# Kernel tuning notes

Hardware: AMD Instinct MI355X
Metric: run time of the kernel (lower is better)

## Reference

```python
import jax, jax.numpy as jnp
from jax import lax
import numpy as np

N_QUBITS = 8
Q_DEPTH = 10
DIM = 256  # 2**8

# basis-state bit table; wire 0 = most-significant bit (PennyLane convention)
_bits = ((np.arange(DIM)[:, None] >> (N_QUBITS - 1 - np.arange(N_QUBITS))) & 1)
# phase layer: S on even wires (phase i), T on odd wires (phase e^{i pi/4})
_ph = np.where(np.arange(N_QUBITS) % 2 == 0, 1j, np.exp(1j * np.pi / 4))
_diag = np.prod(np.power(_ph[None, :], _bits), axis=1)
# entangling_layer_3 CZ pattern
_cz = np.ones(DIM)
for i, j in [(0, 1), (2, 3), (4, 5), (6, 7), (1, 2), (3, 4), (5, 6)]:
    _cz = _cz * ((-1.0) ** (_bits[:, i] * _bits[:, j]))
DIAG = jnp.asarray((_diag * _cz).astype(np.complex64))  # phase+CZ layer fused diagonal
ZSIGNS = jnp.asarray((1 - 2 * _bits).astype(np.float32))  # [256, 8] PauliZ eigenvalues
H_GATE = jnp.asarray((np.array([[1.0, 1.0], [1.0, -1.0]]) / np.sqrt(2.0)).astype(np.complex64))
X_GATE = jnp.asarray(np.array([[0.0, 1.0], [1.0, 0.0]]).astype(np.complex64))
EYE2 = jnp.eye(2, dtype=jnp.complex64)
BN_EPS = 1e-5


def apply_1q(state, U, w):
    """Apply 2x2 gate U on wire w; state: [B, 2,2,...,2]."""
    state = jnp.moveaxis(state, w + 1, -1)
    state = jnp.matmul(state, U.T)
    return jnp.moveaxis(state, -1, w + 1)


def quantum_net(features, q_params):
    """Batched statevector sim of quantum_net_3. features [B,256], q_params [80] -> [B,8]."""
    f = features / jnp.linalg.norm(features, axis=1, keepdims=True)
    state = f.astype(jnp.complex64).reshape((-1,) + (2,) * N_QUBITS)
    for w in range(N_QUBITS):
        state = apply_1q(state, H_GATE, w)
    qw = q_params.reshape(Q_DEPTH, N_QUBITS)
    for layer in range(Q_DEPTH):
        for w in range(N_QUBITS):
            t = qw[layer, w]
            c = jnp.cos(t / 2).astype(jnp.complex64)
            s = jnp.sin(t / 2).astype(jnp.complex64)
            U = c * EYE2 + (-1j) * s * X_GATE  # RX(t)
            state = apply_1q(state, U, w)
        flat = state.reshape(-1, DIM) * DIAG  # phase layer + CZ entangling (diagonal)
        state = flat.reshape((-1,) + (2,) * N_QUBITS)
    sv = state.reshape(-1, DIM)
    probs = sv.real ** 2 + sv.imag ** 2
    return probs @ ZSIGNS  # [B, 8] expval(PauliZ_i)


def conv2d(x, w, b):
    y = lax.conv_general_dilated(x, w, (1, 1), 'SAME', dimension_numbers=('NCHW', 'OIHW', 'NCHW'))
    return y + b[None, :, None, None]


def bn(x, gamma, beta, mean, var):  # eval-mode BatchNorm2d
    inv = gamma / jnp.sqrt(var + BN_EPS)
    return x * inv[None, :, None, None] + (beta - mean * inv)[None, :, None, None]


def maxpool2(x):
    return lax.reduce_window(x, -jnp.inf, lax.max, (1, 1, 2, 2), (1, 1, 2, 2), 'VALID')


def setup_inputs() -> dict:
    key = jax.random.key(0)
    ks = jax.random.split(key, 16)
    B = 1024
    return {
        'x': jax.random.normal(ks[0], (B, 1, 28, 28), dtype=jnp.float32),
        'conv1_w': 0.1 * jax.random.normal(ks[1], (32, 1, 3, 3), dtype=jnp.float32),
        'conv1_b': jnp.zeros((32,), jnp.float32),
        'bn1_gamma': jnp.ones((32,), jnp.float32),
        'bn1_beta': jnp.zeros((32,), jnp.float32),
        'bn1_mean': jnp.zeros((32,), jnp.float32),
        'bn1_var': jnp.ones((32,), jnp.float32),
        'conv2_w': 0.05 * jax.random.normal(ks[2], (64, 32, 3, 3), dtype=jnp.float32),
        'conv2_b': jnp.zeros((64,), jnp.float32),
        'bn2_gamma': jnp.ones((64,), jnp.float32),
        'bn2_beta': jnp.zeros((64,), jnp.float32),
        'bn2_mean': jnp.zeros((64,), jnp.float32),
        'bn2_var': jnp.ones((64,), jnp.float32),
        'fc_w': 0.01 * jax.random.normal(ks[3], (256, 64 * 7 * 7), dtype=jnp.float32),
        'fc_b': jnp.zeros((256,), jnp.float32),
        'q_params': 0.1 * jax.random.normal(ks[4], (Q_DEPTH * N_QUBITS,), dtype=jnp.float32),
        'p1_w': 0.01 * jax.random.normal(ks[5], (128, 8), dtype=jnp.float32),
        'p1_b': jnp.zeros((128,), jnp.float32),
        'p2_w': 0.01 * jax.random.normal(ks[6], (64, 128), dtype=jnp.float32),
        'p2_b': jnp.zeros((64,), jnp.float32),
        'p3_w': 0.01 * jax.random.normal(ks[7], (10, 64), dtype=jnp.float32),
        'p3_b': jnp.zeros((10,), jnp.float32),
    }


def reference(x, conv1_w, conv1_b, bn1_gamma, bn1_beta, bn1_mean, bn1_var,
              conv2_w, conv2_b, bn2_gamma, bn2_beta, bn2_mean, bn2_var,
              fc_w, fc_b, q_params, p1_w, p1_b, p2_w, p2_b, p3_w, p3_b):
    h = maxpool2(jax.nn.relu(bn(conv2d(x, conv1_w, conv1_b), bn1_gamma, bn1_beta, bn1_mean, bn1_var)))
    h = maxpool2(jax.nn.relu(bn(conv2d(h, conv2_w, conv2_b), bn2_gamma, bn2_beta, bn2_mean, bn2_var)))
    h = h.reshape(h.shape[0], -1)  # [B, 64*7*7]
    feats = jnp.tanh(h @ fc_w.T + fc_b)  # [B, 256]
    q = quantum_net(feats, q_params)  # [B, 8]
    z = jax.nn.relu(q @ p1_w.T + p1_b)  # dropout = identity (eval)
    z = jax.nn.relu(z @ p2_w.T + p2_b)
    return z @ p3_w.T + p3_b
```

## Files before the change

kernel.cpp:

```cpp
#include <hip/hip_runtime.h>
#include <math.h>


#define B_SZ 1024

#define OFF_FCWP   0
#define OFF_W2F    802816
#define OFF_SC2    821600
#define OFF_SH2    821664
#define OFF_H1     821728
#define OFF_H2P    7244256

#define KSPLIT_FC 14
#define TS 40

typedef __attribute__((ext_vector_type(8))) short s16x8;
typedef __attribute__((ext_vector_type(4))) float f32x4;

__constant__ float C_COS8[8] = {1.f, 0.70710678f, 0.f, -0.70710678f, -1.f, -0.70710678f, 0.f, 0.70710678f};
__constant__ float C_SIN8[8] = {0.f, 0.70710678f, 1.f, 0.70710678f, 0.f, -0.70710678f, -1.f, -0.70710678f};

__device__ __forceinline__ unsigned short bf16_rne(float f) {
  unsigned u = __float_as_uint(f);
  unsigned r = u + 0x7FFFu + ((u >> 16) & 1u);
  return (unsigned short)(r >> 16);
}
__device__ __forceinline__ int div14(int m) {
  return __float2int_rz((float)m * 0.07142858f);
}

__global__ __launch_bounds__(256) void fused_front_kernel(
    const float* __restrict__ x, const float* __restrict__ c1w, const float* __restrict__ c1b,
    const float* __restrict__ bn1g, const float* __restrict__ bn1b, const float* __restrict__ bn1m,
    const float* __restrict__ bn1v,
    const float* __restrict__ c2w,
    const float* __restrict__ bn2g, const float* __restrict__ bn2b, const float* __restrict__ bn2m,
    const float* __restrict__ bn2v, const float* __restrict__ c2b,
    const float* __restrict__ fc_w,
    float* __restrict__ ws) {
  const int blk = blockIdx.x, tid = threadIdx.x;
  __shared__ float smem[3136];

  if (blk >= 1024) {
    if (blk < 1280) {
      const int n = blk - 1024;
      const float* src = fc_w + n * 3136;
      for (int i = tid; i < 3136; i += 256) smem[i] = src[i];
      __syncthreads();
      unsigned short* us = (unsigned short*)ws;
      const int nt = n >> 4, nl = n & 15;
      for (int k = tid; k < 3136; k += 256) {
        float v = smem[(k & 63) * 49 + (k >> 6)];
        unsigned short hi = bf16_rne(v);
        unsigned short lo = bf16_rne(v - __uint_as_float((unsigned)hi << 16));
        const int lane_ = ((k >> 3) & 3) * 16 + nl;
        const int base = (((k >> 5) * 16 + nt) * 2) * 512 + lane_ * 8 + (k & 7);
        us[base] = hi;
        us[base + 512] = lo;
      }
    } else if (blk < 1424) {
      int g = (blk - 1280) * 256 + tid;
      int j = g & 7, L = (g >> 3) & 63, rest = g >> 9;
      int h = rest & 1; rest >>= 1;
      int t = rest % 9, w = rest / 9;
      int occ = w * 16 + (L & 15);
      int ic  = (L >> 4) * 8 + j;
      float v = c2w[occ * 288 + ic * 9 + t];
      unsigned short hi = bf16_rne(v);
      unsigned short res = hi;
      if (h) res = bf16_rne(v - __uint_as_float((unsigned)hi << 16));
      ((unsigned short*)(ws + OFF_W2F))[g] = res;
    } else {
      if (tid < 64) {
        float inv = bn2g[tid] / sqrtf(bn2v[tid] + 1e-5f);
        ws[OFF_SC2 + tid] = inv;
        ws[OFF_SH2 + tid] = c2b[tid] * inv + bn2b[tid] - bn2m[tid] * inv;
      }
    }
    return;
  }

  const int b = blk;
  float (*xs)[32] = (float (*)[32])smem;
  float* w1s  = smem + 960;
  float* sc1s = smem + 1248;
  float* sh1s = smem + 1280;
  float* h1 = ws + OFF_H1;

  if (tid < 240) ((float4*)smem)[tid] = make_float4(0.f, 0.f, 0.f, 0.f);
  __syncthreads();
  const float* xb = x + b * 784;
  for (int i = tid; i < 784; i += 256) {
    int y = i / 28, c = i - y * 28;
    xs[y + 1][c + 1] = xb[i];
  }
  for (int i = tid; i < 288; i += 256) w1s[i] = c1w[(i & 31) * 9 + (i >> 5)];
  if (tid < 32) {
    float inv = bn1g[tid] / sqrtf(bn1v[tid] + 1e-5f);
    sc1s[tid] = inv;
    sh1s[tid] = c1b[tid] * inv + bn1b[tid] - bn1m[tid] * inv;
  }
  __syncthreads();

  for (int t = tid; t < 448; t += 256) {
    const int oc = t & 31, py = t >> 5;
    float wv[9];
#pragma unroll
    for (int k = 0; k < 9; ++k) wv[k] = w1s[k * 32 + oc];
    float acc0[28], acc1[28];
#pragma unroll
    for (int j = 0; j < 28; ++j) { acc0[j] = 0.f; acc1[j] = 0.f; }
#pragma unroll
    for (int r = 0; r < 4; ++r) {
      const int pr = 2 * py + r;
      float row[32];
#pragma unroll
      for (int q = 0; q < 8; ++q) {
        float4 v = *(const float4*)&xs[pr][4 * q];
        row[4 * q] = v.x; row[4 * q + 1] = v.y; row[4 * q + 2] = v.z; row[4 * q + 3] = v.w;
      }
      if (r <= 2) {
#pragma unroll
        for (int kx = 0; kx < 3; ++kx) {
          const float w = wv[r * 3 + kx];
#pragma unroll
          for (int xx = 0; xx < 28; ++xx) acc0[xx] = fmaf(row[xx + kx], w, acc0[xx]);
        }
      }
      if (r >= 1) {
#pragma unroll
        for (int kx = 0; kx < 3; ++kx) {
          const float w = wv[(r - 1) * 3 + kx];
#pragma unroll
          for (int xx = 0; xx < 28; ++xx) acc1[xx] = fmaf(row[xx + kx], w, acc1[xx]);
        }
      }
    }
    const float sc = sc1s[oc], sh = sh1s[oc];
    float* dst = h1 + b * 6272 + oc * 196 + py * 14;
#pragma unroll
    for (int px = 0; px < 14; ++px) {
      float v0 = fmaxf(fmaf(acc0[2 * px], sc, sh), 0.f);
      float v1 = fmaxf(fmaf(acc0[2 * px + 1], sc, sh), 0.f);
      float v2 = fmaxf(fmaf(acc1[2 * px], sc, sh), 0.f);
      float v3 = fmaxf(fmaf(acc1[2 * px + 1], sc, sh), 0.f);
      dst[px] = fmaxf(fmaxf(v0, v1), fmaxf(v2, v3));
    }
  }
}

__global__ __launch_bounds__(256, 2) void conv2_kernel(
    const float* __restrict__ h1, const float* __restrict__ w2f_f,
    const float* __restrict__ sc2, const float* __restrict__ sh2,
    unsigned short* __restrict__ h2hi, unsigned short* __restrict__ h2lo) {
  const int b = blockIdx.x, tid = threadIdx.x;
  const int lane = tid & 63, w = tid >> 6;

  __shared__ unsigned char lds_raw[50176];
  unsigned short* tile_hi = (unsigned short*)lds_raw;
  unsigned short* tile_lo = (unsigned short*)(lds_raw + 21760);
  float* conv_out = (float*)lds_raw;

  const unsigned short* w2f = (const unsigned short*)w2f_f;
  s16x8 bf[9][2];
#pragma unroll
  for (int t = 0; t < 9; ++t)
#pragma unroll
    for (int h = 0; h < 2; ++h)
      bf[t][h] = *(const s16x8*)&w2f[(((w * 9 + t) * 2 + h) << 9) + lane * 8];

  {
    float4* z = (float4*)lds_raw;
    for (int i = tid; i < 2720; i += 256) z[i] = make_float4(0.f, 0.f, 0.f, 0.f);
  }
  __syncthreads();

  if (tid < 196) {
    const int y = div14(tid), x = tid - y * 14;
    const int sp = ((y + 1) * 16 + (x + 1)) * TS;
    const float* src = h1 + b * 6272 + tid;
#pragma unroll
    for (int c = 0; c < 4; ++c) {
      s16x8 hv, lv;
#pragma unroll
      for (int j = 0; j < 8; ++j) {
        float v = src[(c * 8 + j) * 196];
        unsigned short h16 = bf16_rne(v);
        hv[j] = (short)h16;
        lv[j] = (short)bf16_rne(v - __uint_as_float((unsigned)h16 << 16));
      }
      *(s16x8*)&tile_hi[sp + c * 8] = hv;
      *(s16x8*)&tile_lo[sp + c * 8] = lv;
    }
  }
  __syncthreads();

  f32x4 acc[13];
#pragma unroll
  for (int i = 0; i < 13; ++i) acc[i] = (f32x4){0.f, 0.f, 0.f, 0.f};

  const int kg8 = (lane >> 4) * 8;
#pragma unroll
  for (int mt = 0; mt < 13; ++mt) {
    const int m = mt * 16 + (lane & 15);
    const int y = div14(m), x = m - y * 14;
    const int base = (y * 16 + x) * TS + kg8;
#pragma unroll
    for (int dy = 0; dy < 3; ++dy) {
#pragma unroll
      for (int dx = 0; dx < 3; ++dx) {
        const int off = base + (dy * 16 + dx) * TS;
        s16x8 ah = *(s16x8*)&tile_hi[off];
        s16x8 al = *(s16x8*)&tile_lo[off];
        const int t = dy * 3 + dx;
        acc[mt] = __builtin_amdgcn_mfma_f32_16x16x32_bf16(ah, bf[t][0], acc[mt], 0, 0, 0);
        acc[mt] = __builtin_amdgcn_mfma_f32_16x16x32_bf16(ah, bf[t][1], acc[mt], 0, 0, 0);
        acc[mt] = __builtin_amdgcn_mfma_f32_16x16x32_bf16(al, bf[t][0], acc[mt], 0, 0, 0);
      }
    }
  }
  __syncthreads();

  const int oc = w * 16 + (lane & 15);
  const float sc = sc2[oc], sh = sh2[oc];
  float* cw = conv_out + w * 3136;
#pragma unroll
  for (int mt = 0; mt < 13; ++mt) {
#pragma unroll
    for (int r = 0; r < 4; ++r) {
      const int m = mt * 16 + (lane >> 4) * 4 + r;
      if (m < 196) cw[m * 16 + (lane & 15)] = fmaxf(fmaf(acc[mt][r], sc, sh), 0.f);
    }
  }
  __syncthreads();

#pragma unroll
  for (int i = 0; i < 13; ++i) {
    const int ps = i * 4 + (lane >> 4);
    if (ps < 49) {
      const int py = (ps * 37) >> 8, px = ps - py * 7;
      const int m00 = py * 28 + px * 2;
      const int c0 = m00 * 16 + (lane & 15);
      float v0 = cw[c0], v1 = cw[c0 + 16], v2 = cw[c0 + 224], v3 = cw[c0 + 240];
      float vm = fmaxf(fmaxf(v0, v1), fmaxf(v2, v3));
      unsigned short hv = bf16_rne(vm);
      const int idx = b * 3136 + ps * 64 + oc;
      h2hi[idx] = hv;
      h2lo[idx] = bf16_rne(vm - __uint_as_float((unsigned)hv << 16));
    }
  }
}

__global__ __launch_bounds__(256) void fc_mfma_kernel(
    const unsigned short* __restrict__ h2hi, const unsigned short* __restrict__ h2lo,
    const unsigned short* __restrict__ Bfrag, float* __restrict__ Part) {
  const int tid = threadIdx.x;
  const int lane = tid & 63, w = tid >> 6;
  const int nt0 = blockIdx.x * 4, z = blockIdx.z;
  const int mrow = blockIdx.y * 64 + w * 16 + (lane & 15);
  const int kg8 = (lane >> 4) * 8;
  const unsigned short* arow_hi = h2hi + mrow * 3136 + kg8;
  const unsigned short* arow_lo = h2lo + mrow * 3136 + kg8;

  f32x4 acc[4];
#pragma unroll
  for (int i = 0; i < 4; ++i) acc[i] = (f32x4){0.f, 0.f, 0.f, 0.f};

#pragma unroll
  for (int c = 0; c < 7; ++c) {
    const int kg = z * 7 + c;
    s16x8 ah = *(const s16x8*)(arow_hi + kg * 32);
    s16x8 al = *(const s16x8*)(arow_lo + kg * 32);
#pragma unroll
    for (int nf = 0; nf < 4; ++nf) {
      const unsigned short* bp = Bfrag + (size_t)((kg * 16 + nt0 + nf) * 2) * 512 + lane * 8;
      s16x8 bh = *(const s16x8*)bp;
      s16x8 bl = *(const s16x8*)(bp + 512);
      acc[nf] = __builtin_amdgcn_mfma_f32_16x16x32_bf16(ah, bh, acc[nf], 0, 0, 0);
      acc[nf] = __builtin_amdgcn_mfma_f32_16x16x32_bf16(ah, bl, acc[nf], 0, 0, 0);
      acc[nf] = __builtin_amdgcn_mfma_f32_16x16x32_bf16(al, bh, acc[nf], 0, 0, 0);
    }
  }

  float* dst = Part + (size_t)z * 262144;
  const int mbase = blockIdx.y * 64 + w * 16 + (lane >> 4) * 4;
  const int nbase = (lane & 15);
#pragma unroll
  for (int nf = 0; nf < 4; ++nf) {
#pragma unroll
    for (int r = 0; r < 4; ++r) {
      dst[(mbase + r) * 256 + (nt0 + nf) * 16 + nbase] = acc[nf][r];
    }
  }
}

__global__ __launch_bounds__(256) void quantum_kernel(
    const float* __restrict__ Part, const float* __restrict__ fc_b,
    const float* __restrict__ qp,
    const float* __restrict__ p1w, const float* __restrict__ p1b,
    const float* __restrict__ p2w, const float* __restrict__ p2b,
    const float* __restrict__ p3w, const float* __restrict__ p3b,
    float* __restrict__ out) {
  const int b = blockIdx.x, tid = threadIdx.x;
  __shared__ float2 buf[2][256];
  __shared__ float csl[160];
  __shared__ float part[4][8];
  __shared__ float qv[8];
  __shared__ float z1[128];
  __shared__ float z2s[64];

  if (tid < 80) {
    float t = 0.5f * qp[tid];
    csl[2 * tid] = cosf(t);
    csl[2 * tid + 1] = sinf(t);
  }

  float f = fc_b[tid];
#pragma unroll
  for (int z = 0; z < KSPLIT_FC; ++z) f += Part[z * 262144 + b * 256 + tid];
  f = tanhf(f);

  float ss = f * f;
#pragma unroll
  for (int off = 32; off >= 1; off >>= 1) ss += __shfl_xor(ss, off);
  const int lane = tid & 63, wid = tid >> 6;
  if (lane == 0) part[wid][0] = ss;
  __syncthreads();
  const float tot = part[0][0] + part[1][0] + part[2][0] + part[3][0];
  const float inv = 1.0f / sqrtf(tot);
  float re = f * inv, im = 0.f;

  const int k8 = (2 * __popc(tid & 0xAA) + __popc(tid & 0x55)) & 7;
  float dre = C_COS8[k8], dim_ = C_SIN8[k8];
  {
    const int i = tid;
    int par = ((i >> 7) & (i >> 6)) ^ ((i >> 5) & (i >> 4)) ^ ((i >> 3) & (i >> 2)) ^ ((i >> 1) & i)
            ^ ((i >> 6) & (i >> 5)) ^ ((i >> 4) & (i >> 3)) ^ ((i >> 2) & (i >> 1));
    if (par & 1) { dre = -dre; dim_ = -dim_; }
  }

  int cur = 0;
  const float RS = 0.70710678118654752f;

#pragma unroll
  for (int w = 0; w < 2; ++w) {
    const int m = 128 >> w;
    cur ^= 1;
    buf[cur][tid] = make_float2(re, im);
    __syncthreads();
    float2 p = buf[cur][tid ^ m];
    float sgn = (tid & m) ? -1.f : 1.f;
    re = fmaf(sgn, re, p.x) * RS;
    im = fmaf(sgn, im, p.y) * RS;
  }
#pragma unroll
  for (int w = 2; w < 8; ++w) {
    const int m = 1 << (7 - w);
    float pre = __shfl_xor(re, m);
    float pim = __shfl_xor(im, m);
    float sgn = (tid & m) ? -1.f : 1.f;
    re = fmaf(sgn, re, pre) * RS;
    im = fmaf(sgn, im, pim) * RS;
  }

  for (int layer = 0; layer < 10; ++layer) {
    const float* cs = &csl[16 * layer];
#pragma unroll
    for (int w = 0; w < 2; ++w) {
      const int m = 128 >> w;
      const float c = cs[2 * w], s = cs[2 * w + 1];
      cur ^= 1;
      buf[cur][tid] = make_float2(re, im);
      __syncthreads();
      float2 p = buf[cur][tid ^ m];
      float nre = fmaf(s, p.y, c * re);
      float nim = fmaf(-s, p.x, c * im);
      re = nre; im = nim;
    }
#pragma unroll
    for (int w = 2; w < 8; ++w) {
      const int m = 1 << (7 - w);
      const float c = cs[2 * w], s = cs[2 * w + 1];
      float pre = __shfl_xor(re, m);
      float pim = __shfl_xor(im, m);
      float nre = fmaf(s, pim, c * re);
      float nim = fmaf(-s, pre, c * im);
      if (w == 7) {
        float tre = nre * dre - nim * dim_;
        nim = fmaf(nre, dim_, nim * dre);
        nre = tre;
      }
      re = nre; im = nim;
    }
  }

  const float prb = re * re + im * im;
#pragma unroll
  for (int w = 0; w < 8; ++w) {
    float v = ((tid >> (7 - w)) & 1) ? -prb : prb;
#pragma unroll
    for (int off = 32; off >= 1; off >>= 1) v += __shfl_xor(v, off);
    if (lane == 0) part[wid][w] = v;
  }
  __syncthreads();
  if (tid < 8) qv[tid] = part[0][tid] + part[1][tid] + part[2][tid] + part[3][tid];
  __syncthreads();

  if (tid < 128) {
    float a = p1b[tid];
#pragma unroll
    for (int k = 0; k < 8; ++k) a = fmaf(qv[k], p1w[tid * 8 + k], a);
    z1[tid] = fmaxf(a, 0.f);
  }
  __syncthreads();
  if (tid < 64) {
    float a = p2b[tid];
#pragma unroll 16
    for (int k = 0; k < 128; ++k) a = fmaf(z1[k], p2w[tid * 128 + k], a);
    z2s[tid] = fmaxf(a, 0.f);
  }
  __syncthreads();
  if (tid < 10) {
    float a = p3b[tid];
#pragma unroll 16
    for (int k = 0; k < 64; ++k) a = fmaf(z2s[k], p3w[tid * 64 + k], a);
    out[b * 10 + tid] = a;
  }
}

extern "C" void kernel_launch(void* const* d_in, const int* in_sizes, int n_in,
                              void* d_out, int out_size, void* d_ws, size_t ws_size,
                              hipStream_t stream) {
  (void)in_sizes; (void)n_in; (void)out_size; (void)ws_size;
  const float* x    = (const float*)d_in[0];
  const float* c1w  = (const float*)d_in[1];
  const float* c1b  = (const float*)d_in[2];
  const float* bn1g = (const float*)d_in[3];
  const float* bn1b = (const float*)d_in[4];
  const float* bn1m = (const float*)d_in[5];
  const float* bn1v = (const float*)d_in[6];
  const float* c2w  = (const float*)d_in[7];
  const float* c2b  = (const float*)d_in[8];
  const float* bn2g = (const float*)d_in[9];
  const float* bn2b = (const float*)d_in[10];
  const float* bn2m = (const float*)d_in[11];
  const float* bn2v = (const float*)d_in[12];
  const float* fc_w = (const float*)d_in[13];
  const float* fc_b = (const float*)d_in[14];
  const float* qp   = (const float*)d_in[15];
  const float* p1w  = (const float*)d_in[16];
  const float* p1b  = (const float*)d_in[17];
  const float* p2w  = (const float*)d_in[18];
  const float* p2b  = (const float*)d_in[19];
  const float* p3w  = (const float*)d_in[20];
  const float* p3b  = (const float*)d_in[21];
  float* ws = (float*)d_ws;
  float* outp = (float*)d_out;

  unsigned short* h2hi = (unsigned short*)(ws + OFF_H2P);
  unsigned short* h2lo = h2hi + 3211264;
  const unsigned short* bfrag = (const unsigned short*)ws;

  fused_front_kernel<<<1425, 256, 0, stream>>>(x, c1w, c1b, bn1g, bn1b, bn1m, bn1v,
                                               c2w, bn2g, bn2b, bn2m, bn2v, c2b, fc_w, ws);
  conv2_kernel<<<B_SZ, 256, 0, stream>>>(ws + OFF_H1, ws + OFF_W2F, ws + OFF_SC2, ws + OFF_SH2,
                                         h2hi, h2lo);
  fc_mfma_kernel<<<dim3(4, 16, KSPLIT_FC), 256, 0, stream>>>(h2hi, h2lo, bfrag, ws + OFF_H1);
  quantum_kernel<<<B_SZ, 256, 0, stream>>>(ws + OFF_H1, fc_b, qp, p1w, p1b, p2w, p2b, p3w, p3b, outp);
}
```

Measured before the change: 180.3 us.

## Run quantum simulation in a single wavefront and vectorize fc weight repack stores

The quantum kernel now uses one 64-lane wavefront per sample, each lane holding four amplitudes. The two top-wire gates become in-register butterflies instead of shared-memory exchanges with block barriers, and the reductions and MLP head use wave shuffles rather than shared memory and syncthreads. Separately, the fc weight repack writes eight bf16 values per 128-bit store instead of scalar 16-bit stores. The cost is more registers per lane and fewer threads per block.

```diff
diff --git a/kernel.cpp b/kernel.cpp
--- a/kernel.cpp
+++ b/kernel.cpp
@@ -49,14 +49,21 @@
       __syncthreads();
       unsigned short* us = (unsigned short*)ws;
       const int nt = n >> 4, nl = n & 15;
-      for (int k = tid; k < 3136; k += 256) {
-        float v = smem[(k & 63) * 49 + (k >> 6)];
-        unsigned short hi = bf16_rne(v);
-        unsigned short lo = bf16_rne(v - __uint_as_float((unsigned)hi << 16));
-        const int lane_ = ((k >> 3) & 3) * 16 + nl;
-        const int base = (((k >> 5) * 16 + nt) * 2) * 512 + lane_ * 8 + (k & 7);
-        us[base] = hi;
-        us[base + 512] = lo;
+      for (int idx = tid; idx < 784; idx += 256) {
+        const int part = (idx >= 392);
+        const int rest = idx - part * 392;
+        const int kg = rest >> 2, q = rest & 3;
+        s16x8 v;
+#pragma unroll
+        for (int j = 0; j < 8; ++j) {
+          const int k = kg * 32 + q * 8 + j;
+          float f = smem[(k & 63) * 49 + (k >> 6)];
+          unsigned short hi = bf16_rne(f);
+          unsigned short r = hi;
+          if (part) r = bf16_rne(f - __uint_as_float((unsigned)hi << 16));
+          v[j] = (short)r;
+        }
+        *(s16x8*)&us[((((kg * 16 + nt) * 2 + part)) << 9) + (q * 16 + nl) * 8] = v;
       }
     } else if (blk < 1424) {
       int g = (blk - 1280) * 256 + tid;
@@ -294,137 +301,151 @@
   }
 }
 
-__global__ __launch_bounds__(256) void quantum_kernel(
+__global__ __launch_bounds__(64) void quantum_kernel(
     const float* __restrict__ Part, const float* __restrict__ fc_b,
     const float* __restrict__ qp,
     const float* __restrict__ p1w, const float* __restrict__ p1b,
     const float* __restrict__ p2w, const float* __restrict__ p2b,
     const float* __restrict__ p3w, const float* __restrict__ p3b,
     float* __restrict__ out) {
-  const int b = blockIdx.x, tid = threadIdx.x;
-  __shared__ float2 buf[2][256];
+  const int b = blockIdx.x, lane = threadIdx.x;
   __shared__ float csl[160];
-  __shared__ float part[4][8];
-  __shared__ float qv[8];
-  __shared__ float z1[128];
-  __shared__ float z2s[64];
-
-  if (tid < 80) {
-    float t = 0.5f * qp[tid];
-    csl[2 * tid] = cosf(t);
-    csl[2 * tid + 1] = sinf(t);
-  }
-
-  float f = fc_b[tid];
-#pragma unroll
-  for (int z = 0; z < KSPLIT_FC; ++z) f += Part[z * 262144 + b * 256 + tid];
-  f = tanhf(f);
-
-  float ss = f * f;
+
+  for (int g = lane; g < 80; g += 64) {
+    float t = 0.5f * qp[g];
+    csl[2 * g] = cosf(t);
+    csl[2 * g + 1] = sinf(t);
+  }
+  __syncthreads();
+
+  float fa[4];
+#pragma unroll
+  for (int a = 0; a < 4; ++a) {
+    const int idx = a * 64 + lane;
+    float f = fc_b[idx];
+#pragma unroll
+    for (int z = 0; z < KSPLIT_FC; ++z) f += Part[z * 262144 + b * 256 + idx];
+    fa[a] = tanhf(f);
+  }
+  float ss = fa[0] * fa[0] + fa[1] * fa[1] + fa[2] * fa[2] + fa[3] * fa[3];
 #pragma unroll
   for (int off = 32; off >= 1; off >>= 1) ss += __shfl_xor(ss, off);
-  const int lane = tid & 63, wid = tid >> 6;
-  if (lane == 0) part[wid][0] = ss;
-  __syncthreads();
-  const float tot = part[0][0] + part[1][0] + part[2][0] + part[3][0];
-  const float inv = 1.0f / sqrtf(tot);
-  float re = f * inv, im = 0.f;
-
-  const int k8 = (2 * __popc(tid & 0xAA) + __popc(tid & 0x55)) & 7;
-  float dre = C_COS8[k8], dim_ = C_SIN8[k8];
-  {
-    const int i = tid;
+  const float inv = 1.0f / sqrtf(ss);
+
+  float re[4], im[4];
+#pragma unroll
+  for (int a = 0; a < 4; ++a) { re[a] = fa[a] * inv; im[a] = 0.f; }
+
+  float dre[4], dim_[4];
+#pragma unroll
+  for (int a = 0; a < 4; ++a) {
+    const int i = a * 64 + lane;
+    const int k8 = (2 * __popc(i & 0xAA) + __popc(i & 0x55)) & 7;
+    float dr = C_COS8[k8], di = C_SIN8[k8];
     int par = ((i >> 7) & (i >> 6)) ^ ((i >> 5) & (i >> 4)) ^ ((i >> 3) & (i >> 2)) ^ ((i >> 1) & i)
             ^ ((i >> 6) & (i >> 5)) ^ ((i >> 4) & (i >> 3)) ^ ((i >> 2) & (i >> 1));
-    if (par & 1) { dre = -dre; dim_ = -dim_; }
-  }
-
-  int cur = 0;
+    if (par & 1) { dr = -dr; di = -di; }
+    dre[a] = dr; dim_[a] = di;
+  }
+
   const float RS = 0.70710678118654752f;
 
-#pragma unroll
-  for (int w = 0; w < 2; ++w) {
-    const int m = 128 >> w;
-    cur ^= 1;
-    buf[cur][tid] = make_float2(re, im);
-    __syncthreads();
-    float2 p = buf[cur][tid ^ m];
-    float sgn = (tid & m) ? -1.f : 1.f;
-    re = fmaf(sgn, re, p.x) * RS;
-    im = fmaf(sgn, im, p.y) * RS;
-  }
+#define H_PAIR(u, v)                                        \
+  { float tur = re[u], tui = im[u];                         \
+    re[u] = (tur + re[v]) * RS; im[u] = (tui + im[v]) * RS; \
+    re[v] = (tur - re[v]) * RS; im[v] = (tui - im[v]) * RS; }
+  H_PAIR(0, 2) H_PAIR(1, 3)
+  H_PAIR(0, 1) H_PAIR(2, 3)
 #pragma unroll
   for (int w = 2; w < 8; ++w) {
     const int m = 1 << (7 - w);
-    float pre = __shfl_xor(re, m);
-    float pim = __shfl_xor(im, m);
-    float sgn = (tid & m) ? -1.f : 1.f;
-    re = fmaf(sgn, re, pre) * RS;
-    im = fmaf(sgn, im, pim) * RS;
-  }
-
+    const float sgn = (lane & m) ? -1.f : 1.f;
+#pragma unroll
+    for (int a = 0; a < 4; ++a) {
+      float pre = __shfl_xor(re[a], m);
+      float pim = __shfl_xor(im[a], m);
+      re[a] = fmaf(sgn, re[a], pre) * RS;
+      im[a] = fmaf(sgn, im[a], pim) * RS;
+    }
+  }
+
+#define RX_PAIR(u, v, c, s)                                   \
+  { float ur = re[u], ui = im[u], wr = re[v], wi = im[v];     \
+    re[u] = fmaf(s, wi, c * ur); im[u] = fmaf(-s, wr, c * ui);\
+    re[v] = fmaf(s, ui, c * wr); im[v] = fmaf(-s, ur, c * wi); }
   for (int layer = 0; layer < 10; ++layer) {
     const float* cs = &csl[16 * layer];
-#pragma unroll
-    for (int w = 0; w < 2; ++w) {
-      const int m = 128 >> w;
-      const float c = cs[2 * w], s = cs[2 * w + 1];
-      cur ^= 1;
-      buf[cur][tid] = make_float2(re, im);
-      __syncthreads();
-      float2 p = buf[cur][tid ^ m];
-      float nre = fmaf(s, p.y, c * re);
-      float nim = fmaf(-s, p.x, c * im);
-      re = nre; im = nim;
-    }
+    { const float c = cs[0], s = cs[1]; RX_PAIR(0, 2, c, s) RX_PAIR(1, 3, c, s) }
+    { const float c = cs[2], s = cs[3]; RX_PAIR(0, 1, c, s) RX_PAIR(2, 3, c, s) }
 #pragma unroll
     for (int w = 2; w < 8; ++w) {
       const int m = 1 << (7 - w);
       const float c = cs[2 * w], s = cs[2 * w + 1];
-      float pre = __shfl_xor(re, m);
-      float pim = __shfl_xor(im, m);
-      float nre = fmaf(s, pim, c * re);
-      float nim = fmaf(-s, pre, c * im);
-      if (w == 7) {
-        float tre = nre * dre - nim * dim_;
-        nim = fmaf(nre, dim_, nim * dre);
-        nre = tre;
-      }
-      re = nre; im = nim;
-    }
-  }
-
-  const float prb = re * re + im * im;
+#pragma unroll
+      for (int a = 0; a < 4; ++a) {
+        float pre = __shfl_xor(re[a], m);
+        float pim = __shfl_xor(im[a], m);
+        float nre = fmaf(s, pim, c * re[a]);
+        float nim = fmaf(-s, pre, c * im[a]);
+        if (w == 7) {
+          float tre = nre * dre[a] - nim * dim_[a];
+          nim = fmaf(nre, dim_[a], nim * dre[a]);
+          nre = tre;
+        }
+        re[a] = nre; im[a] = nim;
+      }
+    }
+  }
+
+  float prb[4];
+#pragma unroll
+  for (int a = 0; a < 4; ++a) prb[a] = re[a] * re[a] + im[a] * im[a];
+  float qv[8];
 #pragma unroll
   for (int w = 0; w < 8; ++w) {
-    float v = ((tid >> (7 - w)) & 1) ? -prb : prb;
+    float v;
+    if (w == 0)      v = prb[0] + prb[1] - prb[2] - prb[3];
+    else if (w == 1) v = prb[0] - prb[1] + prb[2] - prb[3];
+    else {
+      const int m = 1 << (7 - w);
+      const float sgn = (lane & m) ? -1.f : 1.f;
+      v = sgn * (prb[0] + prb[1] + prb[2] + prb[3]);
+    }
 #pragma unroll
     for (int off = 32; off >= 1; off >>= 1) v += __shfl_xor(v, off);
-    if (lane == 0) part[wid][w] = v;
-  }
-  __syncthreads();
-  if (tid < 8) qv[tid] = part[0][tid] + part[1][tid] + part[2][tid] + part[3][tid];
-  __syncthreads();
-
-  if (tid < 128) {
-    float a = p1b[tid];
-#pragma unroll
-    for (int k = 0; k < 8; ++k) a = fmaf(qv[k], p1w[tid * 8 + k], a);
-    z1[tid] = fmaxf(a, 0.f);
-  }
-  __syncthreads();
-  if (tid < 64) {
-    float a = p2b[tid];
-#pragma unroll 16
-    for (int k = 0; k < 128; ++k) a = fmaf(z1[k], p2w[tid * 128 + k], a);
-    z2s[tid] = fmaxf(a, 0.f);
-  }
-  __syncthreads();
-  if (tid < 10) {
-    float a = p3b[tid];
-#pragma unroll 16
-    for (int k = 0; k < 64; ++k) a = fmaf(z2s[k], p3w[tid * 64 + k], a);
-    out[b * 10 + tid] = a;
+    qv[w] = v;
+  }
+
+  float z1a = p1b[lane], z1b = p1b[lane + 64];
+#pragma unroll
+  for (int k = 0; k < 8; ++k) {
+    z1a = fmaf(qv[k], p1w[lane * 8 + k], z1a);
+    z1b = fmaf(qv[k], p1w[(lane + 64) * 8 + k], z1b);
+  }
+  z1a = fmaxf(z1a, 0.f); z1b = fmaxf(z1b, 0.f);
+
+  float acc2 = p2b[lane];
+  const float* row2 = p2w + lane * 128;
+#pragma unroll
+  for (int kc = 0; kc < 64; kc += 4) {
+    float4 w0 = *(const float4*)&row2[kc];
+    float4 w1 = *(const float4*)&row2[64 + kc];
+    float wv0[4] = {w0.x, w0.y, w0.z, w0.w};
+    float wv1[4] = {w1.x, w1.y, w1.z, w1.w};
+#pragma unroll
+    for (int j = 0; j < 4; ++j) {
+      acc2 = fmaf(__shfl(z1a, kc + j), wv0[j], acc2);
+      acc2 = fmaf(__shfl(z1b, kc + j), wv1[j], acc2);
+    }
+  }
+  const float z2 = fmaxf(acc2, 0.f);
+
+#pragma unroll
+  for (int n = 0; n < 10; ++n) {
+    float p = z2 * p3w[n * 64 + lane];
+#pragma unroll
+    for (int off = 32; off >= 1; off >>= 1) p += __shfl_xor(p, off);
+    if (lane == n) out[b * 10 + n] = p + p3b[n];
   }
 }
 
@@ -466,5 +487,5 @@
   conv2_kernel<<<B_SZ, 256, 0, stream>>>(ws + OFF_H1, ws + OFF_W2F, ws + OFF_SC2, ws + OFF_SH2,
                                          h2hi, h2lo);
   fc_mfma_kernel<<<dim3(4, 16, KSPLIT_FC), 256, 0, stream>>>(h2hi, h2lo, bfrag, ws + OFF_H1);
-  quantum_kernel<<<B_SZ, 256, 0, stream>>>(ws + OFF_H1, fc_b, qp, p1w, p1b, p2w, p2b, p3w, p3b, outp);
-}
+  quantum_kernel<<<B_SZ, 64, 0, stream>>>(ws + OFF_H1, fc_b, qp, p1w, p1b, p2w, p2b, p3w, p3b, outp);
+}
```

After: 179.5 us. No clear change (-0.4%).
